# Performance work log

Measured on AMD Instinct MI355X. Metric: run time of the kernel, lower is better.

Reference implementation:

```python
import jax, jax.numpy as jnp
import numpy as np

WIN_H, WIN_W = 8, 8
NUM_HEADS = 32


def _relative_position_index(wh: int, ww: int) -> np.ndarray:
    # Swin V1 style pairwise relative position index, [wh*ww, wh*ww]
    coords = np.stack(np.meshgrid(np.arange(wh), np.arange(ww), indexing='ij'))  # [2, wh, ww]
    cf = coords.reshape(2, -1)                      # [2, N]
    rel = cf[:, :, None] - cf[:, None, :]           # [2, N, N]
    rel = rel.transpose(1, 2, 0).copy()             # [N, N, 2]
    rel[:, :, 0] += wh - 1
    rel[:, :, 1] += ww - 1
    rel[:, :, 0] *= 2 * ww - 1
    return rel.sum(-1)                              # [N, N]


def setup_inputs() -> dict:
    key = jax.random.key(0)
    ks = jax.random.split(key, 6)
    B, N, C = 2048, WIN_H * WIN_W, 256
    return {
        'x': jax.random.normal(ks[0], (B, N, C), dtype=jnp.float32),
        'w_qkv': jax.random.normal(ks[1], (3 * C, C), dtype=jnp.float32) * 0.02,
        'b_qkv': jax.random.normal(ks[2], (3 * C,), dtype=jnp.float32) * 0.02,
        'w_proj': jax.random.normal(ks[3], (C, C), dtype=jnp.float32) * 0.02,
        'b_proj': jax.random.normal(ks[4], (C,), dtype=jnp.float32) * 0.02,
        'bias_table': jax.random.normal(ks[5], ((2 * WIN_H - 1) * (2 * WIN_W - 1), NUM_HEADS), dtype=jnp.float32) * 0.02,
    }


def reference(x, w_qkv, b_qkv, w_proj, b_proj, bias_table):
    B, N, C = x.shape
    H = NUM_HEADS
    d = C // H
    idx = jnp.asarray(_relative_position_index(WIN_H, WIN_W).reshape(-1))  # [N*N] int
    # gathered relative positional bias: [H, N, N]
    bias = bias_table[idx].reshape(N, N, H).transpose(2, 0, 1)
    # qkv projection -> [3, B, H, N, d]
    qkv = (x @ w_qkv.T + b_qkv).reshape(B, N, 3, H, d).transpose(2, 0, 3, 1, 4)
    q, k, v = qkv[0], qkv[1], qkv[2]
    # NOTE: torch code normalizes over dim=1 == HEAD axis (faithful quirk),
    # and self.scale is never applied in forward.
    def norm_heads(t):
        n = jnp.sqrt(jnp.sum(t * t, axis=1, keepdims=True))
        return t / jnp.maximum(n, 1e-12)
    q = norm_heads(q)
    k = norm_heads(k)
    logits = jnp.einsum('bhqd,bhkd->bhqk', q, k) + bias[None]  # [B,H,N,N]
    attn = jax.nn.softmax(logits, axis=-1)
    out = jnp.einsum('bhqk,bhkd->bhqd', attn, v)               # [B,H,N,d]
    out = out.transpose(0, 2, 1, 3).reshape(B, N, C)
    return out @ w_proj.T + b_proj
```

## Files before the change

kernel.cpp:

```cpp
#include <hip/hip_runtime.h>

typedef __attribute__((ext_vector_type(4))) float f32x4;
typedef __attribute__((ext_vector_type(8))) short s16x8;
typedef __attribute__((ext_vector_type(4))) short s16x4;

#define NWIN 2048

__device__ __forceinline__ ushort f2bf(float f) {
    union { float f; unsigned u; } v; v.f = f;
    unsigned r = v.u + 0x7FFFu + ((v.u >> 16) & 1u);
    return (ushort)(r >> 16);
}
__device__ __forceinline__ float bf2f(ushort u) {
    union { unsigned u; float f; } v; v.u = ((unsigned)u) << 16;
    return v.f;
}
__device__ __forceinline__ unsigned pk2(float a, float b) {
    return (unsigned)f2bf(a) | ((unsigned)f2bf(b) << 16);
}
union BF4 { unsigned u[2]; unsigned long long ull; s16x4 v; };

__global__ void prep_kernel(const float* __restrict__ wqkv,
                            const float* __restrict__ wproj,
                            const float* __restrict__ btab,
                            ushort* __restrict__ wq,
                            ushort* __restrict__ wp,
                            ushort* __restrict__ bb) {
    int t = blockIdx.x * 256 + threadIdx.x;
    if (t < 196608) {
        wq[t] = f2bf(wqkv[t]);
    } else if (t < 262144) {
        int i = t - 196608;
        wp[i] = f2bf(wproj[i]);
    } else if (t < 393216) {
        int i = t - 262144;
        int h  = i >> 12;
        int rem = i & 4095;
        int qi = rem >> 6;
        int kj = rem & 63;
        int rh = (qi >> 3) - (kj >> 3) + 7;
        int rw = (qi & 7)  - (kj & 7)  + 7;
        bb[i] = f2bf(btab[(rh * 15 + rw) * 32 + h]);
    }
}

__global__ __launch_bounds__(512, 3) void attn_kernel(
    const float* __restrict__ x,
    const float* __restrict__ bqkv,
    const float* __restrict__ bproj,
    const ushort* __restrict__ wq,
    const ushort* __restrict__ wp,
    const ushort* __restrict__ biasb,
    float* __restrict__ out)
{
    __shared__ ushort sX[64 * 256];
    __shared__ ushort sV[32 * 8 * 64];
    __shared__ float  sN[1024];

    const int tid  = threadIdx.x;
    const int lane = tid & 63;
    const int w    = tid >> 6;
    const int g    = lane >> 4;
    const int c    = lane & 15;
    const int b    = blockIdx.x;

    const f32x4 fz = {0.f, 0.f, 0.f, 0.f};
    const s16x4 z4 = {0, 0, 0, 0};

    sN[tid] = 0.f; sN[tid + 512] = 0.f;

    {
        const float4* xg = (const float4*)(x + (size_t)b * 16384);
        #pragma unroll
        for (int it = 0; it < 8; ++it) {
            int i = tid + it * 512;
            float4 v = xg[i];
            int row = i >> 6;
            int col = (i & 63) << 2;
            int bo = (row * 512 + col * 2) ^ ((row & 7) << 4);
            ushort4 u;
            u.x = f2bf(v.x); u.y = f2bf(v.y); u.z = f2bf(v.z); u.w = f2bf(v.w);
            *(ushort4*)((char*)sX + bo) = u;
        }
    }
    __syncthreads();

    {
        f32x4 acc[4][2];
        #pragma unroll
        for (int mi = 0; mi < 4; ++mi) { acc[mi][0] = fz; acc[mi][1] = fz; }
        #pragma unroll
        for (int ks = 0; ks < 8; ++ks) {
            s16x8 af[4];
            #pragma unroll
            for (int mi = 0; mi < 4; ++mi) {
                int row = 16 * mi + c;
                int bo = (row * 512 + ks * 64 + g * 16) ^ ((row & 7) << 4);
                af[mi] = *(const s16x8*)((const char*)sX + bo);
            }
            s16x8 wv[2];
            #pragma unroll
            for (int nj = 0; nj < 2; ++nj)
                wv[nj] = *(const s16x8*)(wq + (512 + 32 * w + 16 * nj + c) * 256 + ks * 32 + g * 8);
            #pragma unroll
            for (int mi = 0; mi < 4; ++mi)
                #pragma unroll
                for (int nj = 0; nj < 2; ++nj)
                    acc[mi][nj] = __builtin_amdgcn_mfma_f32_16x16x32_bf16(af[mi], wv[nj], acc[mi][nj], 0, 0, 0);
        }
        #pragma unroll
        for (int nj = 0; nj < 2; ++nj) {
            int vc = 32 * w + 16 * nj + c;
            float bv = bqkv[512 + vc];
            int hh = vc >> 3, dd = vc & 7;
            #pragma unroll
            for (int mi = 0; mi < 4; ++mi) {
                BF4 t;
                t.u[0] = pk2(acc[mi][nj][0] + bv, acc[mi][nj][1] + bv);
                t.u[1] = pk2(acc[mi][nj][2] + bv, acc[mi][nj][3] + bv);
                int bo = (hh * 1024 + dd * 128 + 32 * mi + 8 * g) ^ (dd << 4);
                *(unsigned long long*)((char*)sV + bo) = t.ull;
            }
        }
    }

    s16x4 kpk[2][4];
    {
        f32x4 ac[2][4];
        #pragma unroll
        for (int mt = 0; mt < 2; ++mt)
            #pragma unroll
            for (int nt = 0; nt < 4; ++nt) ac[mt][nt] = fz;
        #pragma unroll
        for (int ks = 0; ks < 8; ++ks) {
            s16x8 af[4];
            #pragma unroll
            for (int nt = 0; nt < 4; ++nt) {
                int row = 16 * nt + c;
                int bo = (row * 512 + ks * 64 + g * 16) ^ ((row & 7) << 4);
                af[nt] = *(const s16x8*)((const char*)sX + bo);
            }
            s16x8 wk[2];
            #pragma unroll
            for (int mt = 0; mt < 2; ++mt)
                wk[mt] = *(const s16x8*)(wq + (256 + 32 * w + 16 * mt + c) * 256 + ks * 32 + g * 8);
            #pragma unroll
            for (int mt = 0; mt < 2; ++mt)
                #pragma unroll
                for (int nt = 0; nt < 4; ++nt)
                    ac[mt][nt] = __builtin_amdgcn_mfma_f32_16x16x32_bf16(wk[mt], af[nt], ac[mt][nt], 0, 0, 0);
        }
        f32x4 bk0 = *(const f32x4*)(bqkv + 256 + 32 * w + 4 * g);
        f32x4 bk1 = *(const f32x4*)(bqkv + 256 + 32 * w + 16 + 4 * g);
        #pragma unroll
        for (int nt = 0; nt < 4; ++nt) { ac[0][nt] += bk0; ac[1][nt] += bk1; }
        #pragma unroll
        for (int nt = 0; nt < 4; ++nt) {
            #pragma unroll
            for (int j = 0; j < 4; ++j) {
                float p = ac[0][nt][j] * ac[0][nt][j] + ac[1][nt][j] * ac[1][nt][j];
                p += __shfl_xor(p, 32);
                if (g < 2) atomicAdd(&sN[(16 * nt + c) * 8 + 4 * g + j + 512], p);
            }
            #pragma unroll
            for (int mt = 0; mt < 2; ++mt) {
                BF4 t;
                t.u[0] = pk2(ac[mt][nt][0], ac[mt][nt][1]);
                t.u[1] = pk2(ac[mt][nt][2], ac[mt][nt][3]);
                kpk[mt][nt] = t.v;
            }
        }
    }

    s16x4 qpk[2][4];
    {
        f32x4 ac[2][4];
        #pragma unroll
        for (int mt = 0; mt < 2; ++mt)
            #pragma unroll
            for (int nt = 0; nt < 4; ++nt) ac[mt][nt] = fz;
        #pragma unroll
        for (int ks = 0; ks < 8; ++ks) {
            s16x8 af[4];
            #pragma unroll
            for (int nt = 0; nt < 4; ++nt) {
                int row = 16 * nt + c;
                int bo = (row * 512 + ks * 64 + g * 16) ^ ((row & 7) << 4);
                af[nt] = *(const s16x8*)((const char*)sX + bo);
            }
            s16x8 wqa[2];
            #pragma unroll
            for (int mt = 0; mt < 2; ++mt)
                wqa[mt] = *(const s16x8*)(wq + (32 * w + 16 * mt + c) * 256 + ks * 32 + g * 8);
            #pragma unroll
            for (int mt = 0; mt < 2; ++mt)
                #pragma unroll
                for (int nt = 0; nt < 4; ++nt)
                    ac[mt][nt] = __builtin_amdgcn_mfma_f32_16x16x32_bf16(wqa[mt], af[nt], ac[mt][nt], 0, 0, 0);
        }
        f32x4 bq0 = *(const f32x4*)(bqkv + 32 * w + 4 * g);
        f32x4 bq1 = *(const f32x4*)(bqkv + 32 * w + 16 + 4 * g);
        #pragma unroll
        for (int nt = 0; nt < 4; ++nt) { ac[0][nt] += bq0; ac[1][nt] += bq1; }
        #pragma unroll
        for (int nt = 0; nt < 4; ++nt) {
            #pragma unroll
            for (int j = 0; j < 4; ++j) {
                float p = ac[0][nt][j] * ac[0][nt][j] + ac[1][nt][j] * ac[1][nt][j];
                p += __shfl_xor(p, 32);
                if (g < 2) atomicAdd(&sN[(16 * nt + c) * 8 + 4 * g + j], p);
            }
            #pragma unroll
            for (int mt = 0; mt < 2; ++mt) {
                BF4 t;
                t.u[0] = pk2(ac[mt][nt][0], ac[mt][nt][1]);
                t.u[1] = pk2(ac[mt][nt][2], ac[mt][nt][3]);
                qpk[mt][nt] = t.v;
            }
        }
    }
    __syncthreads();

    #pragma unroll
    for (int nt = 0; nt < 4; ++nt) {
        float iq[4], ik[4];
        #pragma unroll
        for (int j = 0; j < 4; ++j) {
            int a = (16 * nt + c) * 8 + ((4 * g + j) & 7);
            iq[j] = 1.f / fmaxf(sqrtf(sN[a]), 1e-12f);
            ik[j] = 1.f / fmaxf(sqrtf(sN[a + 512]), 1e-12f);
        }
        #pragma unroll
        for (int mt = 0; mt < 2; ++mt) {
            BF4 t; t.v = qpk[mt][nt];
            t.u[0] = pk2(bf2f((ushort)(t.u[0] & 0xffff)) * iq[0],
                         bf2f((ushort)(t.u[0] >> 16))    * iq[1]);
            t.u[1] = pk2(bf2f((ushort)(t.u[1] & 0xffff)) * iq[2],
                         bf2f((ushort)(t.u[1] >> 16))    * iq[3]);
            qpk[mt][nt] = t.v;
            t.v = kpk[mt][nt];
            t.u[0] = pk2(bf2f((ushort)(t.u[0] & 0xffff)) * ik[0],
                         bf2f((ushort)(t.u[0] >> 16))    * ik[1]);
            t.u[1] = pk2(bf2f((ushort)(t.u[1] & 0xffff)) * ik[2],
                         bf2f((ushort)(t.u[1] >> 16))    * ik[3]);
            kpk[mt][nt] = t.v;
        }
    }

    #pragma unroll
    for (int hi = 0; hi < 4; ++hi) {
        const int mt = hi >> 1, par = hi & 1, h = 4 * w + hi;
        const bool keepq = par ? (g >= 2) : (g < 2);
        s16x4 vf[4];
        #pragma unroll
        for (int kv = 0; kv < 4; ++kv) {
            if (c < 8) {
                int bo = (h * 1024 + c * 128 + 32 * kv + 8 * g) ^ (c << 4);
                BF4 t; t.ull = *(const unsigned long long*)((const char*)sV + bo);
                vf[kv] = t.v;
            } else vf[kv] = z4;
        }
        const ushort* bh = biasb + h * 4096;
        #pragma unroll
        for (int tq = 0; tq < 4; ++tq) {
            s16x4 qf = keepq ? qpk[mt][tq] : z4;
            f32x4 S[4];
            #pragma unroll
            for (int tk = 0; tk < 4; ++tk)
                S[tk] = __builtin_amdgcn_mfma_f32_16x16x16bf16_1k(kpk[mt][tk], qf, fz, 0, 0, 0);
            float sum = 0.f;
            #pragma unroll
            for (int tk = 0; tk < 4; ++tk) {
                ushort4 bv4 = *(const ushort4*)(bh + (16 * tq + c) * 64 + 16 * tk + 4 * g);
                float e0 = __expf(S[tk][0] + bf2f(bv4.x));
                float e1 = __expf(S[tk][1] + bf2f(bv4.y));
                float e2 = __expf(S[tk][2] + bf2f(bv4.z));
                float e3 = __expf(S[tk][3] + bf2f(bv4.w));
                S[tk][0] = e0; S[tk][1] = e1; S[tk][2] = e2; S[tk][3] = e3;
                sum += e0 + e1 + e2 + e3;
            }
            sum += __shfl_xor(sum, 16);
            sum += __shfl_xor(sum, 32);
            float rinv = 1.f / sum;
            f32x4 o = fz;
            #pragma unroll
            for (int kv = 0; kv < 4; ++kv) {
                BF4 pa;
                pa.u[0] = pk2(S[kv][0] * rinv, S[kv][1] * rinv);
                pa.u[1] = pk2(S[kv][2] * rinv, S[kv][3] * rinv);
                o = __builtin_amdgcn_mfma_f32_16x16x16bf16_1k(pa.v, vf[kv], o, 0, 0, 0);
            }
            if (c < 8) {
                #pragma unroll
                for (int j = 0; j < 4; ++j) {
                    int tok = 16 * tq + 4 * g + j;
                    int bo = (tok * 512 + (h * 8 + c) * 2) ^ ((tok & 7) << 4);
                    *(ushort*)((char*)sX + bo) = f2bf(o[j]);
                }
            }
        }
    }
    __syncthreads();

    {
        f32x4 pacc[4][2];
        #pragma unroll
        for (int mi = 0; mi < 4; ++mi) { pacc[mi][0] = fz; pacc[mi][1] = fz; }
        #pragma unroll
        for (int ks = 0; ks < 8; ++ks) {
            s16x8 af[4];
            #pragma unroll
            for (int mi = 0; mi < 4; ++mi) {
                int row = 16 * mi + c;
                int bo = (row * 512 + ks * 64 + g * 16) ^ ((row & 7) << 4);
                af[mi] = *(const s16x8*)((const char*)sX + bo);
            }
            s16x8 wfr[2];
            #pragma unroll
            for (int nj = 0; nj < 2; ++nj)
                wfr[nj] = *(const s16x8*)(wp + (32 * w + 16 * nj + c) * 256 + ks * 32 + g * 8);
            #pragma unroll
            for (int mi = 0; mi < 4; ++mi)
                #pragma unroll
                for (int nj = 0; nj < 2; ++nj)
                    pacc[mi][nj] = __builtin_amdgcn_mfma_f32_16x16x32_bf16(af[mi], wfr[nj], pacc[mi][nj], 0, 0, 0);
        }
        float* og = out + (size_t)b * 16384;
        #pragma unroll
        for (int nj = 0; nj < 2; ++nj) {
            int col = 32 * w + 16 * nj + c;
            float bp = bproj[col];
            #pragma unroll
            for (int mi = 0; mi < 4; ++mi)
                #pragma unroll
                for (int j = 0; j < 4; ++j)
                    og[(16 * mi + 4 * g + j) * 256 + col] = pacc[mi][nj][j] + bp;
        }
    }
}

extern "C" void kernel_launch(void* const* d_in, const int* in_sizes, int n_in,
                              void* d_out, int out_size, void* d_ws, size_t ws_size,
                              hipStream_t stream) {
    const float* x     = (const float*)d_in[0];
    const float* wqkv  = (const float*)d_in[1];
    const float* bqkv  = (const float*)d_in[2];
    const float* wproj = (const float*)d_in[3];
    const float* bproj = (const float*)d_in[4];
    const float* btab  = (const float*)d_in[5];

    ushort* wq_b   = (ushort*)d_ws;
    ushort* wp_b   = wq_b + 196608;
    ushort* bias_b = wp_b + 65536;

    prep_kernel<<<1536, 256, 0, stream>>>(wqkv, wproj, btab, wq_b, wp_b, bias_b);
    attn_kernel<<<NWIN, 512, 0, stream>>>(x, bqkv, bproj, wq_b, wp_b, bias_b,
                                          (float*)d_out);
}
```

Measured before the change: 444.7 us.

## Keep V in registers via lane shuffles, drop sV LDS, raise occupancy

V projection results now stay in registers, and each head's V fragment is formed with cross-lane shuffles instead of a round trip through an LDS staging buffer. This frees 32 KB of shared memory per block, and the launch bounds rise from 3 to 4 blocks per CU to use that headroom. The float-to-bf16 conversion also switches to the HIP bf16 intrinsics, including a packed two-value conversion. The higher occupancy target puts more pressure on registers, which could cause spills, and the extra live vpk registers add to that pressure.

```diff
diff --git a/kernel.cpp b/kernel.cpp
--- a/kernel.cpp
+++ b/kernel.cpp
@@ -1,4 +1,5 @@
 #include <hip/hip_runtime.h>
+#include <hip/hip_bf16.h>
 
 typedef __attribute__((ext_vector_type(4))) float f32x4;
 typedef __attribute__((ext_vector_type(8))) short s16x8;
@@ -7,16 +8,18 @@
 #define NWIN 2048
 
 __device__ __forceinline__ ushort f2bf(float f) {
-    union { float f; unsigned u; } v; v.f = f;
-    unsigned r = v.u + 0x7FFFu + ((v.u >> 16) & 1u);
-    return (ushort)(r >> 16);
+    union { __hip_bfloat16 h; ushort u; } v;
+    v.h = __float2bfloat16(f);
+    return v.u;
 }
 __device__ __forceinline__ float bf2f(ushort u) {
     union { unsigned u; float f; } v; v.u = ((unsigned)u) << 16;
     return v.f;
 }
 __device__ __forceinline__ unsigned pk2(float a, float b) {
-    return (unsigned)f2bf(a) | ((unsigned)f2bf(b) << 16);
+    union { __hip_bfloat162 h; unsigned u; } v;
+    v.h = __float22bfloat162_rn(make_float2(a, b));
+    return v.u;
 }
 union BF4 { unsigned u[2]; unsigned long long ull; s16x4 v; };
 
@@ -44,7 +47,7 @@
     }
 }
 
-__global__ __launch_bounds__(512, 3) void attn_kernel(
+__global__ __launch_bounds__(512, 4) void attn_kernel(
     const float* __restrict__ x,
     const float* __restrict__ bqkv,
     const float* __restrict__ bproj,
@@ -54,7 +57,6 @@
     float* __restrict__ out)
 {
     __shared__ ushort sX[64 * 256];
-    __shared__ ushort sV[32 * 8 * 64];
     __shared__ float  sN[1024];
 
     const int tid  = threadIdx.x;
@@ -78,13 +80,15 @@
             int row = i >> 6;
             int col = (i & 63) << 2;
             int bo = (row * 512 + col * 2) ^ ((row & 7) << 4);
-            ushort4 u;
-            u.x = f2bf(v.x); u.y = f2bf(v.y); u.z = f2bf(v.z); u.w = f2bf(v.w);
-            *(ushort4*)((char*)sX + bo) = u;
+            uint2 u;
+            u.x = pk2(v.x, v.y);
+            u.y = pk2(v.z, v.w);
+            *(uint2*)((char*)sX + bo) = u;
         }
     }
     __syncthreads();
 
+    s16x4 vpk[4][2];
     {
         f32x4 acc[4][2];
         #pragma unroll
@@ -110,16 +114,13 @@
         }
         #pragma unroll
         for (int nj = 0; nj < 2; ++nj) {
-            int vc = 32 * w + 16 * nj + c;
-            float bv = bqkv[512 + vc];
-            int hh = vc >> 3, dd = vc & 7;
+            float bv = bqkv[512 + 32 * w + 16 * nj + c];
             #pragma unroll
             for (int mi = 0; mi < 4; ++mi) {
                 BF4 t;
                 t.u[0] = pk2(acc[mi][nj][0] + bv, acc[mi][nj][1] + bv);
                 t.u[1] = pk2(acc[mi][nj][2] + bv, acc[mi][nj][3] + bv);
-                int bo = (hh * 1024 + dd * 128 + 32 * mi + 8 * g) ^ (dd << 4);
-                *(unsigned long long*)((char*)sV + bo) = t.ull;
+                vpk[mi][nj] = t.v;
             }
         }
     }
@@ -254,11 +255,12 @@
         s16x4 vf[4];
         #pragma unroll
         for (int kv = 0; kv < 4; ++kv) {
-            if (c < 8) {
-                int bo = (h * 1024 + c * 128 + 32 * kv + 8 * g) ^ (c << 4);
-                BF4 t; t.ull = *(const unsigned long long*)((const char*)sV + bo);
-                vf[kv] = t.v;
-            } else vf[kv] = z4;
+            BF4 t; t.v = vpk[kv][mt];
+            if (par) {
+                t.u[0] = (unsigned)__shfl_xor((int)t.u[0], 8);
+                t.u[1] = (unsigned)__shfl_xor((int)t.u[1], 8);
+            }
+            vf[kv] = (c < 8) ? t.v : z4;
         }
         const ushort* bh = biasb + h * 4096;
         #pragma unroll
```

New measurement: 436.8 us. About the same (-1.8%).
